# Optimization experiments

Hardware: AMD Instinct MI355X
Metric: run time of the kernel (lower is better)

The kernel has to match this reference:

```python
import jax, jax.numpy as jnp
import numpy as np

B, S1, S2, D1, D2 = 4, 2048, 2048, 512, 512
H, DK, DV = 8, 64, 64


def setup_inputs() -> dict:
    key = jax.random.key(0)
    ks = jax.random.split(key, 8)
    x1 = jax.random.normal(ks[0], (B, S1, D1), dtype=jnp.float32)
    x2 = jax.random.normal(ks[1], (B, S2, D2), dtype=jnp.float32)
    x3 = jax.random.normal(ks[2], (B, S2, D2), dtype=jnp.float32)
    s = 0.02
    Wq = jax.random.normal(ks[3], (D1, H * DK), dtype=jnp.float32) * s
    Wk = jax.random.normal(ks[4], (D2, H * DK), dtype=jnp.float32) * s
    Wv = jax.random.normal(ks[5], (D2, H * DV), dtype=jnp.float32) * s
    Wo = jax.random.normal(ks[6], (H * DV, D1), dtype=jnp.float32) * s
    bo = jnp.zeros((D1,), dtype=jnp.float32)
    return {"x1": x1, "x2": x2, "x3": x3, "Wq": Wq, "Wk": Wk, "Wv": Wv, "Wo": Wo, "bo": bo}


def reference(x1, x2, x3, Wq, Wk, Wv, Wo, bo):
    b, s1, _ = x1.shape
    # project to per-head q, k, v: [B, H, S, Dh]
    q = (x1 @ Wq).reshape(b, s1, H, DK).transpose(0, 2, 1, 3)
    k = (x2 @ Wk).reshape(b, x2.shape[1], H, DK).transpose(0, 2, 1, 3)
    v = (x3 @ Wv).reshape(b, x3.shape[1], H, DV).transpose(0, 2, 1, 3)
    scores = jnp.einsum('bhqd,bhkd->bhqk', q, k) / jnp.sqrt(jnp.float32(DK))
    attn = jax.nn.softmax(scores, axis=-1)
    out = jnp.einsum('bhqk,bhkd->bhqd', attn, v)  # [B, H, S1, DV]
    out = out.transpose(0, 2, 1, 3).reshape(b, s1, H * DV)
    return out @ Wo + bo
```

## Files before the change

kernel.cpp:

```cpp
#include <hip/hip_runtime.h>

typedef __attribute__((ext_vector_type(4))) float f32x4;
typedef __attribute__((ext_vector_type(8))) __bf16 bf16x8;
typedef __attribute__((ext_vector_type(4))) __bf16 bf16x4;

#define DEVINL __device__ __forceinline__

DEVINL void gld16(const void* g, void* l) {
  __builtin_amdgcn_global_load_lds((__attribute__((address_space(1))) void*)(void*)g,
                                   (__attribute__((address_space(3))) void*)l, 16, 0, 0);
}


__global__ __launch_bounds__(256) void cvt_x(const float* x1, const float* x2, const float* x3,
                                             __bf16* o0, __bf16* o1, __bf16* o2) {
  const int z = blockIdx.y;
  const float* s = z == 0 ? x1 : z == 1 ? x2 : x3;
  __bf16* d = z == 0 ? o0 : z == 1 ? o1 : o2;
  size_t i = (size_t)blockIdx.x * 256 + threadIdx.x;
  f32x4 v = ((const f32x4*)s)[i];
  bf16x4 o;
#pragma unroll
  for (int j = 0; j < 4; ++j) o[j] = (__bf16)v[j];
  ((bf16x4*)d)[i] = o;
}

__global__ __launch_bounds__(256) void cvt_w(const float* Wq, const float* Wk, const float* Wv,
                                             const float* Wo, __bf16* WT) {
  __shared__ float t[64][65];
  const int z = blockIdx.z;
  const float* W = z == 0 ? Wq : z == 1 ? Wk : z == 2 ? Wv : Wo;
  __bf16* D = WT + (size_t)z * 512 * 512;
  const int r0 = blockIdx.x * 64, c0 = blockIdx.y * 64;
  const int tx = threadIdx.x & 63, ty = threadIdx.x >> 6;
#pragma unroll
  for (int j = 0; j < 16; ++j)
    t[ty + j * 4][tx] = W[(size_t)(r0 + ty + j * 4) * 512 + c0 + tx];
  __syncthreads();
#pragma unroll
  for (int j = 0; j < 16; ++j)
    D[(size_t)(c0 + ty + j * 4) * 512 + r0 + tx] = (__bf16)t[tx][ty + j * 4];
}


DEVINL void gemm_tile(const __bf16* A, const __bf16* Bt, int m0, int n0,
                      __bf16* As, __bf16* Bs, f32x4 acc[4][4]) {
  const int tid = threadIdx.x, lane = tid & 63, w = tid >> 6;
  const int qd = lane >> 4, r = lane & 15;
  const int wm = w & 1, wn = w >> 1;
  const char* ap[2];
  const char* bp[2];
#pragma unroll
  for (int j = 0; j < 2; ++j) {
    int c = (w * 2 + j) * 64 + lane;
    int row = c >> 2, cs = c & 3;
    int gc = cs ^ ((row >> 1) & 3);
    ap[j] = (const char*)(A + (size_t)(m0 + row) * 512 + gc * 8);
    bp[j] = (const char*)(Bt + (size_t)(n0 + row) * 512 + gc * 8);
  }
  int offA[4], offB[4];
#pragma unroll
  for (int t = 0; t < 4; ++t) {
    int m = wm * 64 + t * 16 + r;
    offA[t] = (m * 4 + (qd ^ ((m >> 1) & 3))) * 16;
    int n = wn * 64 + t * 16 + r;
    offB[t] = (n * 4 + (qd ^ ((n >> 1) & 3))) * 16;
  }
  char* AsC = (char*)As;
  char* BsC = (char*)Bs;
  for (int kt = 0; kt < 16; ++kt) {
    __syncthreads();
#pragma unroll
    for (int j = 0; j < 2; ++j) {
      gld16(ap[j] + kt * 64, AsC + (w * 2 + j) * 1024);
      gld16(bp[j] + kt * 64, BsC + (w * 2 + j) * 1024);
    }
    __syncthreads();
    bf16x8 a[4], b[4];
#pragma unroll
    for (int t = 0; t < 4; ++t) {
      a[t] = *(const bf16x8*)(AsC + offA[t]);
      b[t] = *(const bf16x8*)(BsC + offB[t]);
    }
#pragma unroll
    for (int i = 0; i < 4; ++i)
#pragma unroll
      for (int j2 = 0; j2 < 4; ++j2)
        acc[i][j2] = __builtin_amdgcn_mfma_f32_16x16x32_bf16(a[i], b[j2], acc[i][j2], 0, 0, 0);
  }
}

__global__ __launch_bounds__(256, 2) void gemm_proj(const __bf16* x1b, const __bf16* x2b,
                                                    const __bf16* x3b, const __bf16* WT,
                                                    __bf16* Qo, __bf16* Ko, __bf16* Vto) {
  __shared__ __align__(16) __bf16 As[128 * 32];
  __shared__ __align__(16) __bf16 Bs[128 * 32];
  const int z = blockIdx.z;
  const __bf16* A = z == 0 ? x1b : z == 1 ? x2b : x3b;
  const __bf16* Bt = WT + (size_t)z * 512 * 512;
  const int n0 = blockIdx.x * 128, m0 = blockIdx.y * 128;
  f32x4 acc[4][4] = {};
  gemm_tile(A, Bt, m0, n0, As, Bs, acc);
  const int tid = threadIdx.x, lane = tid & 63, w = tid >> 6;
  const int qd = lane >> 4, r = lane & 15, wm = w & 1, wn = w >> 1;
#pragma unroll
  for (int mt = 0; mt < 4; ++mt) {
#pragma unroll
    for (int nt = 0; nt < 4; ++nt) {
      f32x4 v = acc[mt][nt];
      int col = n0 + wn * 64 + nt * 16 + r;
      int h = col >> 6, d = col & 63;
      int mg = m0 + wm * 64 + mt * 16 + qd * 4;
      int b = mg >> 11, s = mg & 2047;
      if (z == 2) {
        bf16x4 pv;
#pragma unroll
        for (int g = 0; g < 4; ++g) pv[g] = (__bf16)v[g];
        *(bf16x4*)(Vto + ((size_t)(b * 8 + h) * 64 + d) * 2048 + s) = pv;
      } else {
        __bf16* O = (z == 0 ? Qo : Ko) + ((size_t)(b * 8 + h) * 2048 + s) * 64 + d;
#pragma unroll
        for (int g = 0; g < 4; ++g) O[(size_t)g * 64] = (__bf16)v[g];
      }
    }
  }
}

__global__ __launch_bounds__(256, 2) void gemm_out(const __bf16* Ob, const __bf16* WoT,
                                                   const float* bo, float* out) {
  __shared__ __align__(16) __bf16 As[128 * 32];
  __shared__ __align__(16) __bf16 Bs[128 * 32];
  const int n0 = blockIdx.x * 128, m0 = blockIdx.y * 128;
  f32x4 acc[4][4] = {};
  gemm_tile(Ob, WoT, m0, n0, As, Bs, acc);
  const int tid = threadIdx.x, lane = tid & 63, w = tid >> 6;
  const int qd = lane >> 4, r = lane & 15, wm = w & 1, wn = w >> 1;
#pragma unroll
  for (int nt = 0; nt < 4; ++nt) {
    int col = n0 + wn * 64 + nt * 16 + r;
    float bv = bo[col];
#pragma unroll
    for (int mt = 0; mt < 4; ++mt) {
      int mg = m0 + wm * 64 + mt * 16 + qd * 4;
#pragma unroll
      for (int g = 0; g < 4; ++g) out[(size_t)(mg + g) * 512 + col] = acc[mt][nt][g] + bv;
    }
  }
}

__global__ __launch_bounds__(256, 2) void attn(const __bf16* Q, const __bf16* K,
                                               const __bf16* Vt, __bf16* O) {
  __shared__ __align__(16) __bf16 Qs[128 * 64];
  __shared__ __align__(16) __bf16 Ks[64 * 64];
  __shared__ __align__(16) __bf16 Vs[64 * 64];
  __shared__ __align__(16) __bf16 Ps[128 * 72];
  const int tid = threadIdx.x, lane = tid & 63, w = tid >> 6;
  const int qd = lane >> 4, r = lane & 15;
  const int bh = blockIdx.y;
  const int q0 = blockIdx.x * 128;
  const __bf16* Qg = Q + ((size_t)bh * 2048 + q0) * 64;
  const __bf16* Kg = K + (size_t)bh * 2048 * 64;
  const __bf16* Vg = Vt + (size_t)bh * 64 * 2048;
  char* QsC = (char*)Qs;
  char* KsC = (char*)Ks;
  char* VsC = (char*)Vs;
  char* PsC = (char*)Ps;

#pragma unroll
  for (int j = 0; j < 4; ++j) {
    int c = (w * 4 + j) * 64 + lane;
    int m = c >> 3, cs = c & 7, gc = cs ^ (m & 7);
    gld16((const char*)Qg + m * 128 + gc * 16, QsC + (w * 4 + j) * 1024);
  }
  __syncthreads();

  bf16x8 qf[2][2];
#pragma unroll
  for (int mt = 0; mt < 2; ++mt)
#pragma unroll
    for (int ks = 0; ks < 2; ++ks) {
      int m = w * 32 + mt * 16 + r;
      qf[mt][ks] = *(const bf16x8*)(QsC + m * 128 + ((ks * 4 + qd) ^ (m & 7)) * 16);
    }

  int offKV[4][2];
#pragma unroll
  for (int t = 0; t < 4; ++t)
#pragma unroll
    for (int ks = 0; ks < 2; ++ks) {
      int n = t * 16 + r;
      offKV[t][ks] = n * 128 + ((ks * 4 + qd) ^ (n & 7)) * 16;
    }

  f32x4 oacc[2][4] = {};
  float lpart[2][4] = {};

  for (int kt = 0; kt < 32; ++kt) {
    __syncthreads();
#pragma unroll
    for (int j = 0; j < 2; ++j) {
      int c = (w * 2 + j) * 64 + lane;
      int m = c >> 3, cs = c & 7, gc = cs ^ (m & 7);
      gld16((const char*)Kg + ((size_t)(kt * 64 + m) * 64 + gc * 8) * 2, KsC + (w * 2 + j) * 1024);
      gld16((const char*)Vg + ((size_t)m * 2048 + kt * 64 + gc * 8) * 2, VsC + (w * 2 + j) * 1024);
    }
    __syncthreads();

    f32x4 sf[2][4] = {};
#pragma unroll
    for (int nt = 0; nt < 4; ++nt) {
      bf16x8 kf0 = *(const bf16x8*)(KsC + offKV[nt][0]);
      bf16x8 kf1 = *(const bf16x8*)(KsC + offKV[nt][1]);
#pragma unroll
      for (int mt = 0; mt < 2; ++mt) {
        sf[mt][nt] = __builtin_amdgcn_mfma_f32_16x16x32_bf16(qf[mt][0], kf0, sf[mt][nt], 0, 0, 0);
        sf[mt][nt] = __builtin_amdgcn_mfma_f32_16x16x32_bf16(qf[mt][1], kf1, sf[mt][nt], 0, 0, 0);
      }
    }
#pragma unroll
    for (int mt = 0; mt < 2; ++mt) {
      int rowbase = w * 32 + mt * 16 + qd * 4;
#pragma unroll
      for (int nt = 0; nt < 4; ++nt) {
#pragma unroll
        for (int g = 0; g < 4; ++g) {
          float p = __expf(sf[mt][nt][g] * 0.125f);
          lpart[mt][g] += p;
          Ps[(rowbase + g) * 72 + nt * 16 + r] = (__bf16)p;
        }
      }
    }
#pragma unroll
    for (int mt = 0; mt < 2; ++mt) {
      int prow = w * 32 + mt * 16 + r;
      bf16x8 pf0 = *(const bf16x8*)(PsC + prow * 144 + qd * 16);
      bf16x8 pf1 = *(const bf16x8*)(PsC + prow * 144 + 64 + qd * 16);
#pragma unroll
      for (int dvt = 0; dvt < 4; ++dvt) {
        bf16x8 vf0 = *(const bf16x8*)(VsC + offKV[dvt][0]);
        bf16x8 vf1 = *(const bf16x8*)(VsC + offKV[dvt][1]);
        oacc[mt][dvt] = __builtin_amdgcn_mfma_f32_16x16x32_bf16(pf0, vf0, oacc[mt][dvt], 0, 0, 0);
        oacc[mt][dvt] = __builtin_amdgcn_mfma_f32_16x16x32_bf16(pf1, vf1, oacc[mt][dvt], 0, 0, 0);
      }
    }
  }

  const int b = bh >> 3, h = bh & 7;
#pragma unroll
  for (int mt = 0; mt < 2; ++mt) {
#pragma unroll
    for (int g = 0; g < 4; ++g) {
      float l = lpart[mt][g];
      l += __shfl_xor(l, 1, 64);
      l += __shfl_xor(l, 2, 64);
      l += __shfl_xor(l, 4, 64);
      l += __shfl_xor(l, 8, 64);
      float inv = 1.0f / l;
      int s = q0 + w * 32 + mt * 16 + qd * 4 + g;
#pragma unroll
      for (int dvt = 0; dvt < 4; ++dvt)
        O[((size_t)b * 2048 + s) * 512 + h * 64 + dvt * 16 + r] =
            (__bf16)(oacc[mt][dvt][g] * inv);
    }
  }
}


extern "C" void kernel_launch(void* const* d_in, const int* in_sizes, int n_in,
                              void* d_out, int out_size, void* d_ws, size_t ws_size,
                              hipStream_t stream) {
  const float* x1 = (const float*)d_in[0];
  const float* x2 = (const float*)d_in[1];
  const float* x3 = (const float*)d_in[2];
  const float* Wq = (const float*)d_in[3];
  const float* Wk = (const float*)d_in[4];
  const float* Wv = (const float*)d_in[5];
  const float* Wo = (const float*)d_in[6];
  const float* bo = (const float*)d_in[7];
  float* out = (float*)d_out;
  char* ws = (char*)d_ws;
  const size_t MB = 1ull << 20;
  __bf16* x1b = (__bf16*)(ws);
  __bf16* x2b = (__bf16*)(ws + 8 * MB);
  __bf16* x3b = (__bf16*)(ws + 16 * MB);
  __bf16* WT = (__bf16*)(ws + 24 * MB);
  __bf16* Qb = (__bf16*)(ws + 26 * MB);
  __bf16* Kb = (__bf16*)(ws + 34 * MB);
  __bf16* Vtb = (__bf16*)(ws + 42 * MB);
  __bf16* Ob = (__bf16*)(ws + 50 * MB);

  cvt_x<<<dim3(4096, 3), 256, 0, stream>>>(x1, x2, x3, x1b, x2b, x3b);
  cvt_w<<<dim3(8, 8, 4), 256, 0, stream>>>(Wq, Wk, Wv, Wo, WT);
  gemm_proj<<<dim3(4, 64, 3), 256, 0, stream>>>(x1b, x2b, x3b, WT, Qb, Kb, Vtb);
  attn<<<dim3(16, 32), 256, 0, stream>>>(Qb, Kb, Vtb, Ob);
  gemm_out<<<dim3(4, 64), 256, 0, stream>>>(Ob, WT + 3ull * 512 * 512, bo, out);
}
```

Before: 206.4 us.

## Double-buffer attention K/V loads, widen GEMM K-tile, remap blocks for XCD locality

The attention kernel now double-buffers K and V tiles in LDS. It prefetches the next tile while computing on the current one, which cuts the per-iteration barriers to one. The shared GEMM tile routine doubles its K step from 32 to 64 with a new 8-way XOR swizzle, halving loop trips and barriers at the cost of more LDS. All three compute kernels switch to a 1D grid with a remapped block index, so consecutive blocks landing on the same XCD share heads or row panels for better L2 reuse. Risks include higher LDS use reducing occupancy and relying on the barrier to drain the async LDS loads.

```diff
diff --git a/kernel.cpp b/kernel.cpp
--- a/kernel.cpp
+++ b/kernel.cpp
@@ -48,57 +48,65 @@
   const int tid = threadIdx.x, lane = tid & 63, w = tid >> 6;
   const int qd = lane >> 4, r = lane & 15;
   const int wm = w & 1, wn = w >> 1;
-  const char* ap[2];
-  const char* bp[2];
-#pragma unroll
-  for (int j = 0; j < 2; ++j) {
-    int c = (w * 2 + j) * 64 + lane;
-    int row = c >> 2, cs = c & 3;
-    int gc = cs ^ ((row >> 1) & 3);
-    ap[j] = (const char*)(A + (size_t)(m0 + row) * 512 + gc * 8);
-    bp[j] = (const char*)(Bt + (size_t)(n0 + row) * 512 + gc * 8);
-  }
-  int offA[4], offB[4];
-#pragma unroll
-  for (int t = 0; t < 4; ++t) {
-    int m = wm * 64 + t * 16 + r;
-    offA[t] = (m * 4 + (qd ^ ((m >> 1) & 3))) * 16;
-    int n = wn * 64 + t * 16 + r;
-    offB[t] = (n * 4 + (qd ^ ((n >> 1) & 3))) * 16;
-  }
+  const char* ap[4];
+  const char* bp[4];
+#pragma unroll
+  for (int j = 0; j < 4; ++j) {
+    int c = (w * 4 + j) * 64 + lane;
+    int row = c >> 3, cs = c & 7;
+    int gc = cs ^ (row & 7);
+    ap[j] = (const char*)A + (size_t)(m0 + row) * 1024 + gc * 16;
+    bp[j] = (const char*)Bt + (size_t)(n0 + row) * 1024 + gc * 16;
+  }
+  int offA[4][2], offB[4][2];
+#pragma unroll
+  for (int t = 0; t < 4; ++t)
+#pragma unroll
+    for (int ks = 0; ks < 2; ++ks) {
+      int m = wm * 64 + t * 16 + r;
+      offA[t][ks] = m * 128 + (((ks * 4 + qd) ^ (m & 7)) * 16);
+      int n = wn * 64 + t * 16 + r;
+      offB[t][ks] = n * 128 + (((ks * 4 + qd) ^ (n & 7)) * 16);
+    }
   char* AsC = (char*)As;
   char* BsC = (char*)Bs;
-  for (int kt = 0; kt < 16; ++kt) {
+  for (int kt = 0; kt < 8; ++kt) {
     __syncthreads();
 #pragma unroll
-    for (int j = 0; j < 2; ++j) {
-      gld16(ap[j] + kt * 64, AsC + (w * 2 + j) * 1024);
-      gld16(bp[j] + kt * 64, BsC + (w * 2 + j) * 1024);
+    for (int j = 0; j < 4; ++j) {
+      gld16(ap[j] + kt * 128, AsC + (w * 4 + j) * 1024);
+      gld16(bp[j] + kt * 128, BsC + (w * 4 + j) * 1024);
     }
     __syncthreads();
-    bf16x8 a[4], b[4];
-#pragma unroll
-    for (int t = 0; t < 4; ++t) {
-      a[t] = *(const bf16x8*)(AsC + offA[t]);
-      b[t] = *(const bf16x8*)(BsC + offB[t]);
-    }
-#pragma unroll
-    for (int i = 0; i < 4; ++i)
-#pragma unroll
-      for (int j2 = 0; j2 < 4; ++j2)
-        acc[i][j2] = __builtin_amdgcn_mfma_f32_16x16x32_bf16(a[i], b[j2], acc[i][j2], 0, 0, 0);
+#pragma unroll
+    for (int ks = 0; ks < 2; ++ks) {
+      bf16x8 a[4], b[4];
+#pragma unroll
+      for (int t = 0; t < 4; ++t) {
+        a[t] = *(const bf16x8*)(AsC + offA[t][ks]);
+        b[t] = *(const bf16x8*)(BsC + offB[t][ks]);
+      }
+#pragma unroll
+      for (int i = 0; i < 4; ++i)
+#pragma unroll
+        for (int j2 = 0; j2 < 4; ++j2)
+          acc[i][j2] = __builtin_amdgcn_mfma_f32_16x16x32_bf16(a[i], b[j2], acc[i][j2], 0, 0, 0);
+    }
   }
 }
 
 __global__ __launch_bounds__(256, 2) void gemm_proj(const __bf16* x1b, const __bf16* x2b,
                                                     const __bf16* x3b, const __bf16* WT,
                                                     __bf16* Qo, __bf16* Ko, __bf16* Vto) {
-  __shared__ __align__(16) __bf16 As[128 * 32];
-  __shared__ __align__(16) __bf16 Bs[128 * 32];
+  __shared__ __align__(16) __bf16 As[128 * 64];
+  __shared__ __align__(16) __bf16 Bs[128 * 64];
   const int z = blockIdx.z;
   const __bf16* A = z == 0 ? x1b : z == 1 ? x2b : x3b;
   const __bf16* Bt = WT + (size_t)z * 512 * 512;
-  const int n0 = blockIdx.x * 128, m0 = blockIdx.y * 128;
+  const int l = blockIdx.x;
+  const int sidx = l >> 3;
+  const int m0 = ((l & 7) * 8 + (sidx >> 2)) * 128;
+  const int n0 = (sidx & 3) * 128;
   f32x4 acc[4][4] = {};
   gemm_tile(A, Bt, m0, n0, As, Bs, acc);
   const int tid = threadIdx.x, lane = tid & 63, w = tid >> 6;
@@ -128,9 +136,12 @@
 
 __global__ __launch_bounds__(256, 2) void gemm_out(const __bf16* Ob, const __bf16* WoT,
                                                    const float* bo, float* out) {
-  __shared__ __align__(16) __bf16 As[128 * 32];
-  __shared__ __align__(16) __bf16 Bs[128 * 32];
-  const int n0 = blockIdx.x * 128, m0 = blockIdx.y * 128;
+  __shared__ __align__(16) __bf16 As[128 * 64];
+  __shared__ __align__(16) __bf16 Bs[128 * 64];
+  const int l = blockIdx.x;
+  const int sidx = l >> 3;
+  const int m0 = ((l & 7) * 8 + (sidx >> 2)) * 128;
+  const int n0 = (sidx & 3) * 128;
   f32x4 acc[4][4] = {};
   gemm_tile(Ob, WoT, m0, n0, As, Bs, acc);
   const int tid = threadIdx.x, lane = tid & 63, w = tid >> 6;
@@ -151,13 +162,14 @@
 __global__ __launch_bounds__(256, 2) void attn(const __bf16* Q, const __bf16* K,
                                                const __bf16* Vt, __bf16* O) {
   __shared__ __align__(16) __bf16 Qs[128 * 64];
-  __shared__ __align__(16) __bf16 Ks[64 * 64];
-  __shared__ __align__(16) __bf16 Vs[64 * 64];
+  __shared__ __align__(16) __bf16 Ks[2][64 * 64];
+  __shared__ __align__(16) __bf16 Vs[2][64 * 64];
   __shared__ __align__(16) __bf16 Ps[128 * 72];
   const int tid = threadIdx.x, lane = tid & 63, w = tid >> 6;
   const int qd = lane >> 4, r = lane & 15;
-  const int bh = blockIdx.y;
-  const int q0 = blockIdx.x * 128;
+  const int id = blockIdx.x;
+  const int bh = (id & 7) * 4 + ((id >> 3) >> 4);
+  const int q0 = ((id >> 3) & 15) * 128;
   const __bf16* Qg = Q + ((size_t)bh * 2048 + q0) * 64;
   const __bf16* Kg = K + (size_t)bh * 2048 * 64;
   const __bf16* Vg = Vt + (size_t)bh * 64 * 2048;
@@ -172,6 +184,13 @@
     int m = c >> 3, cs = c & 7, gc = cs ^ (m & 7);
     gld16((const char*)Qg + m * 128 + gc * 16, QsC + (w * 4 + j) * 1024);
   }
+#pragma unroll
+  for (int j = 0; j < 2; ++j) {
+    int c = (w * 2 + j) * 64 + lane;
+    int m = c >> 3, cs = c & 7, gc = cs ^ (m & 7);
+    gld16((const char*)Kg + (size_t)m * 128 + gc * 16, KsC + (w * 2 + j) * 1024);
+    gld16((const char*)Vg + (size_t)m * 4096 + gc * 16, VsC + (w * 2 + j) * 1024);
+  }
   __syncthreads();
 
   bf16x8 qf[2][2];
@@ -196,21 +215,26 @@
   float lpart[2][4] = {};
 
   for (int kt = 0; kt < 32; ++kt) {
-    __syncthreads();
-#pragma unroll
-    for (int j = 0; j < 2; ++j) {
-      int c = (w * 2 + j) * 64 + lane;
-      int m = c >> 3, cs = c & 7, gc = cs ^ (m & 7);
-      gld16((const char*)Kg + ((size_t)(kt * 64 + m) * 64 + gc * 8) * 2, KsC + (w * 2 + j) * 1024);
-      gld16((const char*)Vg + ((size_t)m * 2048 + kt * 64 + gc * 8) * 2, VsC + (w * 2 + j) * 1024);
-    }
-    __syncthreads();
+    const int cur = kt & 1;
+    if (kt < 31) {
+#pragma unroll
+      for (int j = 0; j < 2; ++j) {
+        int c = (w * 2 + j) * 64 + lane;
+        int m = c >> 3, cs = c & 7, gc = cs ^ (m & 7);
+        gld16((const char*)Kg + (size_t)((kt + 1) * 64 + m) * 128 + gc * 16,
+              KsC + (cur ^ 1) * 8192 + (w * 2 + j) * 1024);
+        gld16((const char*)Vg + (size_t)m * 4096 + (kt + 1) * 128 + gc * 16,
+              VsC + (cur ^ 1) * 8192 + (w * 2 + j) * 1024);
+      }
+    }
+    const char* Kb = KsC + cur * 8192;
+    const char* Vb = VsC + cur * 8192;
 
     f32x4 sf[2][4] = {};
 #pragma unroll
     for (int nt = 0; nt < 4; ++nt) {
-      bf16x8 kf0 = *(const bf16x8*)(KsC + offKV[nt][0]);
-      bf16x8 kf1 = *(const bf16x8*)(KsC + offKV[nt][1]);
+      bf16x8 kf0 = *(const bf16x8*)(Kb + offKV[nt][0]);
+      bf16x8 kf1 = *(const bf16x8*)(Kb + offKV[nt][1]);
 #pragma unroll
       for (int mt = 0; mt < 2; ++mt) {
         sf[mt][nt] = __builtin_amdgcn_mfma_f32_16x16x32_bf16(qf[mt][0], kf0, sf[mt][nt], 0, 0, 0);
@@ -237,12 +261,13 @@
       bf16x8 pf1 = *(const bf16x8*)(PsC + prow * 144 + 64 + qd * 16);
 #pragma unroll
       for (int dvt = 0; dvt < 4; ++dvt) {
-        bf16x8 vf0 = *(const bf16x8*)(VsC + offKV[dvt][0]);
-        bf16x8 vf1 = *(const bf16x8*)(VsC + offKV[dvt][1]);
+        bf16x8 vf0 = *(const bf16x8*)(Vb + offKV[dvt][0]);
+        bf16x8 vf1 = *(const bf16x8*)(Vb + offKV[dvt][1]);
         oacc[mt][dvt] = __builtin_amdgcn_mfma_f32_16x16x32_bf16(pf0, vf0, oacc[mt][dvt], 0, 0, 0);
         oacc[mt][dvt] = __builtin_amdgcn_mfma_f32_16x16x32_bf16(pf1, vf1, oacc[mt][dvt], 0, 0, 0);
       }
     }
+    __syncthreads();
   }
 
   const int b = bh >> 3, h = bh & 7;
@@ -291,7 +316,7 @@
 
   cvt_x<<<dim3(4096, 3), 256, 0, stream>>>(x1, x2, x3, x1b, x2b, x3b);
   cvt_w<<<dim3(8, 8, 4), 256, 0, stream>>>(Wq, Wk, Wv, Wo, WT);
-  gemm_proj<<<dim3(4, 64, 3), 256, 0, stream>>>(x1b, x2b, x3b, WT, Qb, Kb, Vtb);
-  attn<<<dim3(16, 32), 256, 0, stream>>>(Qb, Kb, Vtb, Ob);
-  gemm_out<<<dim3(4, 64), 256, 0, stream>>>(Ob, WT + 3ull * 512 * 512, bo, out);
-}
+  gemm_proj<<<dim3(256, 1, 3), 256, 0, stream>>>(x1b, x2b, x3b, WT, Qb, Kb, Vtb);
+  attn<<<dim3(512), 256, 0, stream>>>(Qb, Kb, Vtb, Ob);
+  gemm_out<<<dim3(256), 256, 0, stream>>>(Ob, WT + 3ull * 512 * 512, bo, out);
+}
```

Measured after the change: 207.0 us. Within noise of the previous version (+0.3%).
